# Performance work log

Measured on AMD Instinct MI355X. Metric: run time of the kernel, lower is better.

## Reference

```python
import jax, jax.numpy as jnp
import numpy as np

MAX_DEPTH = 7
DEPTH_SIZES = [4 ** d for d in range(1, MAX_DEPTH + 1)]  # nodes per depth
N_NODES = sum(DEPTH_SIZES)  # 21844
N_TIMES = 48
HIDDEN = 1024
ENC_DIM = 256
B, S = 128, 32


def setup_inputs() -> dict:
    key = jax.random.key(0)
    k = jax.random.split(key, 6)
    return {
        "prefix_embedding": jax.random.normal(k[0], (B, S, HIDDEN), dtype=jnp.float32),
        "emb_matrix": jax.random.normal(k[1], (N_NODES, ENC_DIM), dtype=jnp.float32) * 0.02,
        "W_key": jax.random.normal(k[2], (HIDDEN, ENC_DIM), dtype=jnp.float32) * (1.0 / np.sqrt(ENC_DIM)),
        "b_key": jax.random.normal(k[3], (HIDDEN,), dtype=jnp.float32) * 0.01,
        "W_time": jax.random.normal(k[4], (N_TIMES, HIDDEN), dtype=jnp.float32) * (1.0 / np.sqrt(HIDDEN)),
        "b_time": jax.random.normal(k[5], (N_TIMES,), dtype=jnp.float32) * 0.01,
    }


def reference(prefix_embedding, emb_matrix, W_key, b_key, W_time, b_time):
    # keys = embedding_to_key(make_embedding_matrix(...)): [N_NODES, HIDDEN]
    keys = emb_matrix @ W_key.T + b_key
    # bmm(prefix [B,S,H], keys^T): keys identical across batch -> shared einsum
    scores = jnp.einsum("bsh,nh->bsn", prefix_embedding, keys)  # [B,S,N_NODES]
    # multitask: per-depth gather of the contiguous node block + log_softmax
    locations = []
    off = 0
    for n in DEPTH_SIZES:
        locations.append(jax.nn.log_softmax(scores[..., off:off + n], axis=-1))
        off += n
    time = jax.nn.log_softmax(prefix_embedding @ W_time.T + b_time, axis=-1)  # [B,S,N_TIMES]
    return tuple(locations) + (time,)
```

## Files before the change

kernel.cpp:

```cpp
#include <hip/hip_runtime.h>

#define NNODES 21844
#define ENC 256
#define HID 1024
#define ROWS 4096
#define NTIMES 48

typedef __attribute__((ext_vector_type(8))) short bf16x8;
typedef __attribute__((ext_vector_type(8))) unsigned short u16x8;
typedef __attribute__((ext_vector_type(4))) float f32x4;

__device__ const int g_off[8] = {0, 4, 20, 84, 340, 1364, 5460, 21844};

__device__ inline unsigned short f2bf(float f) {
  unsigned int u = __float_as_uint(f);
  u += 0x7FFF + ((u >> 16) & 1);
  return (unsigned short)(u >> 16);
}

__device__ inline int depth_of(int c) {
  return (c >= 4) + (c >= 20) + (c >= 84) + (c >= 340) + (c >= 1364) + (c >= 5460);
}

__global__ __launch_bounds__(256) void prep(const float* __restrict__ prefix,
                                            const float* __restrict__ emb,
                                            const float* __restrict__ Wk,
                                            const float* __restrict__ Wt,
                                            unsigned short* __restrict__ Pb16,
                                            unsigned short* __restrict__ Eb,
                                            unsigned short* __restrict__ WkT,
                                            float* __restrict__ WtT,
                                            float* __restrict__ S) {
  int bid = blockIdx.x, tid = threadIdx.x;
  if (bid < 4096) {
    int i = bid * 256 + tid;
    float4 v = reinterpret_cast<const float4*>(prefix)[i];
    ushort4 o; o.x = f2bf(v.x); o.y = f2bf(v.y); o.z = f2bf(v.z); o.w = f2bf(v.w);
    reinterpret_cast<ushort4*>(Pb16)[i] = o;
  } else if (bid < 9557) {
    int i = (bid - 4096) * 256 + tid;
    float4 v = reinterpret_cast<const float4*>(emb)[i];
    ushort4 o; o.x = f2bf(v.x); o.y = f2bf(v.y); o.z = f2bf(v.z); o.w = f2bf(v.w);
    reinterpret_cast<ushort4*>(Eb)[i] = o;
  } else if (bid < 10581) {
    int i = (bid - 9557) * 256 + tid;
    int e = i >> 10, h = i & 1023;
    WkT[i] = f2bf(Wk[h * ENC + e]);
  } else if (bid < 10773) {
    int i = (bid - 10581) * 256 + tid;
    int k = i / NTIMES, c = i % NTIMES;
    WtT[i] = Wt[c * HID + k];
  } else {
    int i = (bid - 10773) * 256 + tid;
    reinterpret_cast<float4*>(S)[i] = float4{0.f, 0.f, 0.f, 0.f};
  }
}

__global__ __launch_bounds__(256) void p2_mfma(const unsigned short* __restrict__ Ab,
                                               const unsigned short* __restrict__ Bb,
                                               unsigned short* __restrict__ P2) {
  int lane = threadIdx.x & 63, w = threadIdx.x >> 6;
  int lr = lane & 15, lg = lane >> 4;
  int m0 = blockIdx.y * 64 + w * 16;
  int nb = blockIdx.x * 64;
  f32x4 acc[4];
#pragma unroll
  for (int n = 0; n < 4; ++n) acc[n] = f32x4{0.f, 0.f, 0.f, 0.f};
  const unsigned short* Ap = Ab + (long)(m0 + lr) * HID + lg * 8;
  for (int kk = 0; kk < 32; ++kk) {
    bf16x8 a = *reinterpret_cast<const bf16x8*>(Ap + kk * 32);
#pragma unroll
    for (int n = 0; n < 4; ++n) {
      bf16x8 b = *reinterpret_cast<const bf16x8*>(Bb + (long)(nb + n * 16 + lr) * HID + kk * 32 + lg * 8);
      acc[n] = __builtin_amdgcn_mfma_f32_16x16x32_bf16(a, b, acc[n], 0, 0, 0);
    }
  }
#pragma unroll
  for (int n = 0; n < 4; ++n)
#pragma unroll
    for (int j = 0; j < 4; ++j)
      P2[(m0 + lg * 4 + j) * ENC + nb + n * 16 + lr] = f2bf(acc[n][j]);
}

template <int BF16S>
__global__ __launch_bounds__(256) void gemm_stash(const unsigned short* __restrict__ P2,
                                                  const unsigned short* __restrict__ E,
                                                  unsigned short* __restrict__ stash,
                                                  float* __restrict__ outp,
                                                  float* __restrict__ S) {
  __shared__ unsigned short SH[2][2][128 * 64];
  int tid = threadIdx.x;
  int lane = tid & 63, w = tid >> 6;
  int lr = lane & 15, lg = lane >> 4;
  int wr = w >> 1, wc = w & 1;
  int m0 = blockIdx.x * 128, n0 = blockIdx.y * 128;
  int rr = tid >> 3, c8 = tid & 7;

  f32x4 acc[4][4];
#pragma unroll
  for (int m = 0; m < 4; ++m)
#pragma unroll
    for (int n = 0; n < 4; ++n) acc[m][n] = f32x4{0.f, 0.f, 0.f, 0.f};

#define STAGE(buf, kt)                                                                    \
  _Pragma("unroll") for (int r = 0; r < 4; ++r) {                                         \
    const unsigned short* ga = P2 + (long)(m0 + r * 32 + rr) * ENC + (kt) * 64 + c8 * 8;  \
    __builtin_amdgcn_global_load_lds(                                                     \
        (const __attribute__((address_space(1))) unsigned int*)ga,                        \
        (__attribute__((address_space(3))) unsigned int*)(&SH[buf][0][r * 2048 + w * 512]), \
        16, 0, 0);                                                                        \
    int er = n0 + r * 32 + rr;                                                            \
    if (er > NNODES - 1) er = NNODES - 1;                                                 \
    const unsigned short* gb = E + (long)er * ENC + (kt) * 64 + c8 * 8;                   \
    __builtin_amdgcn_global_load_lds(                                                     \
        (const __attribute__((address_space(1))) unsigned int*)gb,                        \
        (__attribute__((address_space(3))) unsigned int*)(&SH[buf][1][r * 2048 + w * 512]), \
        16, 0, 0);                                                                        \
  }

  STAGE(0, 0)
  __syncthreads();
  for (int kt = 0; kt < 4; ++kt) {
    int cur = kt & 1;
    if (kt < 3) { STAGE(cur ^ 1, kt + 1) }
    const unsigned short* As = &SH[cur][0][0];
    const unsigned short* Bs = &SH[cur][1][0];
#pragma unroll
    for (int kk = 0; kk < 2; ++kk) {
      bf16x8 a[4], b[4];
#pragma unroll
      for (int m = 0; m < 4; ++m)
        a[m] = *reinterpret_cast<const bf16x8*>(As + (wr * 64 + m * 16 + lr) * 64 + kk * 32 + lg * 8);
#pragma unroll
      for (int n = 0; n < 4; ++n)
        b[n] = *reinterpret_cast<const bf16x8*>(Bs + (wc * 64 + n * 16 + lr) * 64 + kk * 32 + lg * 8);
#pragma unroll
      for (int m = 0; m < 4; ++m)
#pragma unroll
        for (int n = 0; n < 4; ++n)
          acc[m][n] = __builtin_amdgcn_mfma_f32_16x16x32_bf16(a[m], b[n], acc[m][n], 0, 0, 0);
    }
    __syncthreads();
  }
#undef STAGE

  int rbase = m0 + wr * 64 + lg * 4;
  int hstart = n0 + wc * 64;
#pragma unroll
  for (int n = 0; n < 4; ++n) {
    int gc = hstart + n * 16 + lr;
    if (gc < NNODES) {
      int d = depth_of(gc);
      long ob = ((long)g_off[d] << 12) + (gc - g_off[d]);
      int sh = 2 * (d + 1);
#pragma unroll
      for (int m = 0; m < 4; ++m)
#pragma unroll
        for (int j = 0; j < 4; ++j) {
          int row = rbase + m * 16 + j;
          long idx = ob + ((long)row << sh);
          if (BF16S) stash[idx] = f2bf(acc[m][n][j]);
          else       outp[idx]  = acc[m][n][j];
        }
    }
  }
  int dlo = depth_of(hstart);
  int hend = hstart + 63; if (hend > NNODES - 1) hend = NNODES - 1;
  int dhi = depth_of(hend);
  int cd[4];
#pragma unroll
  for (int n = 0; n < 4; ++n) {
    int gc = hstart + n * 16 + lr;
    cd[n] = (gc < NNODES) ? depth_of(gc) : 99;
  }
#pragma unroll
  for (int m = 0; m < 4; ++m)
#pragma unroll
    for (int n = 0; n < 4; ++n)
#pragma unroll
      for (int j = 0; j < 4; ++j) acc[m][n][j] = __expf(acc[m][n][j]);
  for (int dt = dlo; dt <= dhi; ++dt) {
#pragma unroll
    for (int m = 0; m < 4; ++m) {
      float s[4] = {0.f, 0.f, 0.f, 0.f};
#pragma unroll
      for (int n = 0; n < 4; ++n) {
        bool use = (cd[n] == dt);
#pragma unroll
        for (int j = 0; j < 4; ++j) s[j] += use ? acc[m][n][j] : 0.f;
      }
#pragma unroll
      for (int j = 0; j < 4; ++j)
#pragma unroll
        for (int o = 1; o < 16; o <<= 1) s[j] += __shfl_xor(s[j], o);
      if (lr == 0) {
#pragma unroll
        for (int j = 0; j < 4; ++j)
          atomicAdd(&S[dt * ROWS + rbase + m * 16 + j], s[j]);
      }
    }
  }
}

template <int BF16S>
__global__ __launch_bounds__(256) void sub_write(const unsigned short* __restrict__ stash,
                                                 const float* __restrict__ S,
                                                 float* __restrict__ out,
                                                 const float* __restrict__ prefix,
                                                 const float* __restrict__ WtT,
                                                 const float* __restrict__ bt) {
  if (blockIdx.x >= 43688) {
    int lane = threadIdx.x & 63;
    int row = (blockIdx.x - 43688) * 4 + (threadIdx.x >> 6);
    const float4* pr = reinterpret_cast<const float4*>(prefix + (long)row * HID);
    float acc = -3.4e38f;
    if (lane < NTIMES) {
      float a = 0.f;
#pragma unroll 4
      for (int q = 0; q < HID / 4; ++q) {
        float4 pv = pr[q];
        const float* wrow = WtT + q * 4 * NTIMES;
        a += pv.x * wrow[lane] + pv.y * wrow[NTIMES + lane] +
             pv.z * wrow[2 * NTIMES + lane] + pv.w * wrow[3 * NTIMES + lane];
      }
      acc = a + bt[lane];
    }
    float m = acc;
#pragma unroll
    for (int d = 32; d; d >>= 1) m = fmaxf(m, __shfl_xor(m, d));
    float e = (lane < NTIMES) ? __expf(acc - m) : 0.f;
    float s = e;
#pragma unroll
    for (int d = 32; d; d >>= 1) s += __shfl_xor(s, d);
    if (lane < NTIMES)
      __builtin_nontemporal_store(acc - m - __logf(s), out + 89473024 + row * NTIMES + lane);
    return;
  }
  long base = (long)blockIdx.x * 2048 + threadIdx.x * 8;
  int d = (base >= 16384) + (base >= 81920) + (base >= 344064) +
          (base >= 1392640) + (base >= 5586944) + (base >= 22364160);
  long bd = (d == 0) ? 0L : (d == 1) ? 16384L : (d == 2) ? 81920L : (d == 3) ? 344064L
          : (d == 4) ? 1392640L : (d == 5) ? 5586944L : 22364160L;
  long rel = base - bd;
  const float* sp = S + d * ROWS;
  float v[8];
  if (BF16S) {
    u16x8 u = *reinterpret_cast<const u16x8*>(stash + base);
#pragma unroll
    for (int j = 0; j < 8; ++j) v[j] = __uint_as_float((unsigned)(unsigned short)u[j] << 16);
  } else {
    float4 a = reinterpret_cast<const float4*>(out + base)[0];
    float4 b = reinterpret_cast<const float4*>(out + base)[1];
    v[0] = a.x; v[1] = a.y; v[2] = a.z; v[3] = a.w;
    v[4] = b.x; v[5] = b.y; v[6] = b.z; v[7] = b.w;
  }
  f32x4 o0, o1;
  if (d == 0) {
    int r0 = (int)(rel >> 2);
    float l0 = __logf(sp[r0]), l1 = __logf(sp[r0 + 1]);
    o0 = f32x4{v[0] - l0, v[1] - l0, v[2] - l0, v[3] - l0};
    o1 = f32x4{v[4] - l1, v[5] - l1, v[6] - l1, v[7] - l1};
  } else {
    int row = (int)(rel >> (2 * (d + 1)));
    float l = __logf(sp[row]);
    o0 = f32x4{v[0] - l, v[1] - l, v[2] - l, v[3] - l};
    o1 = f32x4{v[4] - l, v[5] - l, v[6] - l, v[7] - l};
  }
  f32x4* op = reinterpret_cast<f32x4*>(out + base);
  __builtin_nontemporal_store(o0, op);
  __builtin_nontemporal_store(o1, op + 1);
}

extern "C" void kernel_launch(void* const* d_in, const int* in_sizes, int n_in,
                              void* d_out, int out_size, void* d_ws, size_t ws_size,
                              hipStream_t stream) {
  const float* prefix = (const float*)d_in[0];
  const float* emb    = (const float*)d_in[1];
  const float* Wk     = (const float*)d_in[2];
  const float* Wt     = (const float*)d_in[4];
  const float* bt     = (const float*)d_in[5];
  float* out = (float*)d_out;
  char* ws = (char*)d_ws;

  unsigned short* P2    = (unsigned short*)(ws + 0);
  unsigned short* Eb    = (unsigned short*)(ws + 2097152);
  unsigned short* WkT   = (unsigned short*)(ws + 13281280);
  unsigned short* Pb16  = (unsigned short*)(ws + 13805568);
  float*          WtT   = (float*)(ws + 22194176);
  float*          S     = (float*)(ws + 22390784);
  unsigned short* stash = (unsigned short*)(ws + 22505472);
  const size_t WS_NEED_STASH = 22505472UL + 178946048UL;

  bool big = ws_size >= WS_NEED_STASH;

  prep<<<10801, 256, 0, stream>>>(prefix, emb, Wk, Wt, Pb16, Eb, WkT, WtT, S);

  p2_mfma<<<dim3(4, 64), 256, 0, stream>>>(Pb16, WkT, P2);

  if (big) {
    gemm_stash<1><<<dim3(32, 171), 256, 0, stream>>>(P2, Eb, stash, out, S);
    sub_write<1><<<44712, 256, 0, stream>>>(stash, S, out, prefix, WtT, bt);
  } else {
    gemm_stash<0><<<dim3(32, 171), 256, 0, stream>>>(P2, Eb, stash, out, S);
    sub_write<0><<<44712, 256, 0, stream>>>(stash, S, out, prefix, WtT, bt);
  }
}
```

Measured before the change: 362.7 us.

## Stage GEMM tile through LDS for coalesced stash stores; persistent sub_write grid

Measured after the change: 385.0 us. 1.06x slower.

```diff
diff --git a/kernel.cpp b/kernel.cpp
--- a/kernel.cpp
+++ b/kernel.cpp
@@ -8,6 +8,7 @@
 
 typedef __attribute__((ext_vector_type(8))) short bf16x8;
 typedef __attribute__((ext_vector_type(8))) unsigned short u16x8;
+typedef __attribute__((ext_vector_type(4))) unsigned short u16x4;
 typedef __attribute__((ext_vector_type(4))) float f32x4;
 
 __device__ const int g_off[8] = {0, 4, 20, 84, 340, 1364, 5460, 21844};
@@ -144,60 +145,97 @@
   }
 #undef STAGE
 
-  int rbase = m0 + wr * 64 + lg * 4;
-  int hstart = n0 + wc * 64;
-#pragma unroll
-  for (int n = 0; n < 4; ++n) {
-    int gc = hstart + n * 16 + lr;
-    if (gc < NNODES) {
-      int d = depth_of(gc);
-      long ob = ((long)g_off[d] << 12) + (gc - g_off[d]);
-      int sh = 2 * (d + 1);
-#pragma unroll
-      for (int m = 0; m < 4; ++m)
-#pragma unroll
-        for (int j = 0; j < 4; ++j) {
-          int row = rbase + m * 16 + j;
-          long idx = ob + ((long)row << sh);
-          if (BF16S) stash[idx] = f2bf(acc[m][n][j]);
-          else       outp[idx]  = acc[m][n][j];
+  int hend = n0 + 127; if (hend > NNODES - 1) hend = NNODES - 1;
+  int d0 = depth_of(n0), d1 = depth_of(hend);
+  bool fast = BF16S && (d0 == d1) && (d0 >= 3) && (n0 + 128 <= NNODES);
+
+  unsigned short* T = &SH[0][0][0];
+  int rl0 = wr * 64 + lg * 4;
+  int cl0 = wc * 64 + lr;
+#pragma unroll
+  for (int n = 0; n < 4; ++n)
+#pragma unroll
+    for (int m = 0; m < 4; ++m)
+#pragma unroll
+      for (int j = 0; j < 4; ++j) {
+        int rl = rl0 + m * 16 + j, cl = cl0 + n * 16;
+        T[rl * 128 + (cl ^ ((rl & 7) << 3))] = f2bf(acc[m][n][j]);
+      }
+
+  if (!fast) {
+    int rbase = m0 + rl0;
+#pragma unroll
+    for (int n = 0; n < 4; ++n) {
+      int gc = n0 + cl0 + n * 16;
+      if (gc < NNODES) {
+        int d = depth_of(gc);
+        long ob = ((long)g_off[d] << 12) + (gc - g_off[d]);
+        int sh = 2 * (d + 1);
+#pragma unroll
+        for (int m = 0; m < 4; ++m)
+#pragma unroll
+          for (int j = 0; j < 4; ++j) {
+            int row = rbase + m * 16 + j;
+            long idx = ob + ((long)row << sh);
+            if (BF16S) stash[idx] = f2bf(acc[m][n][j]);
+            else       outp[idx]  = acc[m][n][j];
+          }
+      }
+    }
+  }
+
+  {
+    int rbase = m0 + rl0;
+    int hstart = n0 + wc * 64;
+    int dlo = depth_of(hstart);
+    int he2 = hstart + 63; if (he2 > NNODES - 1) he2 = NNODES - 1;
+    int dhi = depth_of(he2);
+    int cd[4];
+#pragma unroll
+    for (int n = 0; n < 4; ++n) {
+      int gc = hstart + n * 16 + lr;
+      cd[n] = (gc < NNODES) ? depth_of(gc) : 99;
+    }
+#pragma unroll
+    for (int m = 0; m < 4; ++m)
+#pragma unroll
+      for (int n = 0; n < 4; ++n)
+#pragma unroll
+        for (int j = 0; j < 4; ++j) acc[m][n][j] = __expf(acc[m][n][j]);
+    for (int dt = dlo; dt <= dhi; ++dt) {
+#pragma unroll
+      for (int m = 0; m < 4; ++m) {
+        float s[4] = {0.f, 0.f, 0.f, 0.f};
+#pragma unroll
+        for (int n = 0; n < 4; ++n) {
+          bool use = (cd[n] == dt);
+#pragma unroll
+          for (int j = 0; j < 4; ++j) s[j] += use ? acc[m][n][j] : 0.f;
         }
-    }
-  }
-  int dlo = depth_of(hstart);
-  int hend = hstart + 63; if (hend > NNODES - 1) hend = NNODES - 1;
-  int dhi = depth_of(hend);
-  int cd[4];
-#pragma unroll
-  for (int n = 0; n < 4; ++n) {
-    int gc = hstart + n * 16 + lr;
-    cd[n] = (gc < NNODES) ? depth_of(gc) : 99;
-  }
-#pragma unroll
-  for (int m = 0; m < 4; ++m)
-#pragma unroll
-    for (int n = 0; n < 4; ++n)
-#pragma unroll
-      for (int j = 0; j < 4; ++j) acc[m][n][j] = __expf(acc[m][n][j]);
-  for (int dt = dlo; dt <= dhi; ++dt) {
-#pragma unroll
-    for (int m = 0; m < 4; ++m) {
-      float s[4] = {0.f, 0.f, 0.f, 0.f};
-#pragma unroll
-      for (int n = 0; n < 4; ++n) {
-        bool use = (cd[n] == dt);
-#pragma unroll
-        for (int j = 0; j < 4; ++j) s[j] += use ? acc[m][n][j] : 0.f;
+#pragma unroll
+        for (int j = 0; j < 4; ++j)
+#pragma unroll
+          for (int o = 1; o < 16; o <<= 1) s[j] += __shfl_xor(s[j], o);
+        if (lr == 0) {
+#pragma unroll
+          for (int j = 0; j < 4; ++j)
+            atomicAdd(&S[dt * ROWS + rbase + m * 16 + j], s[j]);
+        }
       }
-#pragma unroll
-      for (int j = 0; j < 4; ++j)
-#pragma unroll
-        for (int o = 1; o < 16; o <<= 1) s[j] += __shfl_xor(s[j], o);
-      if (lr == 0) {
-#pragma unroll
-        for (int j = 0; j < 4; ++j)
-          atomicAdd(&S[dt * ROWS + rbase + m * 16 + j], s[j]);
-      }
+    }
+  }
+
+  __syncthreads();
+  if (fast) {
+    int off = g_off[d0];
+    long nd = 4L << (2 * d0);
+    int row = tid >> 1, seg = (tid & 1) * 64;
+    long idx = ((long)ROWS) * off + (long)(m0 + row) * nd + (n0 - off) + seg;
+    u16x4* dst = reinterpret_cast<u16x4*>(stash + idx);
+#pragma unroll
+    for (int q = 0; q < 16; ++q) {
+      int col = (seg + q * 4) ^ ((row & 7) << 3);
+      dst[q] = *reinterpret_cast<const u16x4*>(&T[row * 128 + col]);
     }
   }
 }
@@ -209,66 +247,70 @@
                                                  const float* __restrict__ prefix,
                                                  const float* __restrict__ WtT,
                                                  const float* __restrict__ bt) {
-  if (blockIdx.x >= 43688) {
-    int lane = threadIdx.x & 63;
-    int row = (blockIdx.x - 43688) * 4 + (threadIdx.x >> 6);
-    const float4* pr = reinterpret_cast<const float4*>(prefix + (long)row * HID);
-    float acc = -3.4e38f;
-    if (lane < NTIMES) {
-      float a = 0.f;
-#pragma unroll 4
-      for (int q = 0; q < HID / 4; ++q) {
-        float4 pv = pr[q];
-        const float* wrow = WtT + q * 4 * NTIMES;
-        a += pv.x * wrow[lane] + pv.y * wrow[NTIMES + lane] +
-             pv.z * wrow[2 * NTIMES + lane] + pv.w * wrow[3 * NTIMES + lane];
+  int tid = threadIdx.x;
+  if (blockIdx.x < 256) {
+    int lane = tid & 63, w = tid >> 6;
+#pragma unroll
+    for (int r4 = 0; r4 < 4; ++r4) {
+      int row = blockIdx.x * 16 + w * 4 + r4;
+      const float4* pr = reinterpret_cast<const float4*>(prefix + (long)row * HID);
+      float acc = -3.4e38f;
+      if (lane < NTIMES) {
+        float a0 = 0.f, a1 = 0.f, a2 = 0.f, a3 = 0.f;
+        for (int q = 0; q < HID / 4; ++q) {
+          float4 pv = pr[q];
+          const float* wrow = WtT + q * 4 * NTIMES;
+          a0 += pv.x * wrow[lane];
+          a1 += pv.y * wrow[NTIMES + lane];
+          a2 += pv.z * wrow[2 * NTIMES + lane];
+          a3 += pv.w * wrow[3 * NTIMES + lane];
+        }
+        acc = (a0 + a1) + (a2 + a3) + bt[lane];
       }
-      acc = a + bt[lane];
-    }
-    float m = acc;
-#pragma unroll
-    for (int d = 32; d; d >>= 1) m = fmaxf(m, __shfl_xor(m, d));
-    float e = (lane < NTIMES) ? __expf(acc - m) : 0.f;
-    float s = e;
-#pragma unroll
-    for (int d = 32; d; d >>= 1) s += __shfl_xor(s, d);
-    if (lane < NTIMES)
-      __builtin_nontemporal_store(acc - m - __logf(s), out + 89473024 + row * NTIMES + lane);
+      float m = acc;
+#pragma unroll
+      for (int d = 32; d; d >>= 1) m = fmaxf(m, __shfl_xor(m, d));
+      float e = (lane < NTIMES) ? __expf(acc - m) : 0.f;
+      float s = e;
+#pragma unroll
+      for (int d = 32; d; d >>= 1) s += __shfl_xor(s, d);
+      if (lane < NTIMES) out[89473024 + row * NTIMES + lane] = acc - m - __logf(s);
+    }
     return;
   }
-  long base = (long)blockIdx.x * 2048 + threadIdx.x * 8;
-  int d = (base >= 16384) + (base >= 81920) + (base >= 344064) +
-          (base >= 1392640) + (base >= 5586944) + (base >= 22364160);
-  long bd = (d == 0) ? 0L : (d == 1) ? 16384L : (d == 2) ? 81920L : (d == 3) ? 344064L
-          : (d == 4) ? 1392640L : (d == 5) ? 5586944L : 22364160L;
-  long rel = base - bd;
-  const float* sp = S + d * ROWS;
-  float v[8];
-  if (BF16S) {
-    u16x8 u = *reinterpret_cast<const u16x8*>(stash + base);
-#pragma unroll
-    for (int j = 0; j < 8; ++j) v[j] = __uint_as_float((unsigned)(unsigned short)u[j] << 16);
-  } else {
-    float4 a = reinterpret_cast<const float4*>(out + base)[0];
-    float4 b = reinterpret_cast<const float4*>(out + base)[1];
-    v[0] = a.x; v[1] = a.y; v[2] = a.z; v[3] = a.w;
-    v[4] = b.x; v[5] = b.y; v[6] = b.z; v[7] = b.w;
-  }
-  f32x4 o0, o1;
-  if (d == 0) {
-    int r0 = (int)(rel >> 2);
-    float l0 = __logf(sp[r0]), l1 = __logf(sp[r0 + 1]);
-    o0 = f32x4{v[0] - l0, v[1] - l0, v[2] - l0, v[3] - l0};
-    o1 = f32x4{v[4] - l1, v[5] - l1, v[6] - l1, v[7] - l1};
-  } else {
-    int row = (int)(rel >> (2 * (d + 1)));
-    float l = __logf(sp[row]);
-    o0 = f32x4{v[0] - l, v[1] - l, v[2] - l, v[3] - l};
-    o1 = f32x4{v[4] - l, v[5] - l, v[6] - l, v[7] - l};
-  }
-  f32x4* op = reinterpret_cast<f32x4*>(out + base);
-  __builtin_nontemporal_store(o0, op);
-  __builtin_nontemporal_store(o1, op + 1);
+  for (int c = (int)blockIdx.x - 256; c < 43688; c += 2048) {
+    long base = (long)c * 2048 + tid * 8;
+    int d = (c >= 8) + (c >= 40) + (c >= 168) + (c >= 680) + (c >= 2728) + (c >= 10920);
+    long bd = (d == 0) ? 0L : (d == 1) ? 16384L : (d == 2) ? 81920L : (d == 3) ? 344064L
+            : (d == 4) ? 1392640L : (d == 5) ? 5586944L : 22364160L;
+    long rel = base - bd;
+    const float* sp = S + d * ROWS;
+    float v[8];
+    if (BF16S) {
+      u16x8 u = *reinterpret_cast<const u16x8*>(stash + base);
+#pragma unroll
+      for (int j = 0; j < 8; ++j) v[j] = __uint_as_float((unsigned)(unsigned short)u[j] << 16);
+    } else {
+      float4 a = reinterpret_cast<const float4*>(out + base)[0];
+      float4 b = reinterpret_cast<const float4*>(out + base)[1];
+      v[0] = a.x; v[1] = a.y; v[2] = a.z; v[3] = a.w;
+      v[4] = b.x; v[5] = b.y; v[6] = b.z; v[7] = b.w;
+    }
+    float4 o0, o1;
+    if (d == 0) {
+      int r0 = (int)(rel >> 2);
+      float l0 = __logf(sp[r0]), l1 = __logf(sp[r0 + 1]);
+      o0 = float4{v[0] - l0, v[1] - l0, v[2] - l0, v[3] - l0};
+      o1 = float4{v[4] - l1, v[5] - l1, v[6] - l1, v[7] - l1};
+    } else {
+      int row = (int)(rel >> (2 * (d + 1)));
+      float l = __logf(sp[row]);
+      o0 = float4{v[0] - l, v[1] - l, v[2] - l, v[3] - l};
+      o1 = float4{v[4] - l, v[5] - l, v[6] - l, v[7] - l};
+    }
+    reinterpret_cast<float4*>(out + base)[0] = o0;
+    reinterpret_cast<float4*>(out + base)[1] = o1;
+  }
 }
 
 extern "C" void kernel_launch(void* const* d_in, const int* in_sizes, int n_in,
@@ -299,9 +341,9 @@
 
   if (big) {
     gemm_stash<1><<<dim3(32, 171), 256, 0, stream>>>(P2, Eb, stash, out, S);
-    sub_write<1><<<44712, 256, 0, stream>>>(stash, S, out, prefix, WtT, bt);
+    sub_write<1><<<2304, 256, 0, stream>>>(stash, S, out, prefix, WtT, bt);
   } else {
     gemm_stash<0><<<dim3(32, 171), 256, 0, stream>>>(P2, Eb, stash, out, S);
-    sub_write<0><<<44712, 256, 0, stream>>>(stash, S, out, prefix, WtT, bt);
-  }
-}
+    sub_write<0><<<2304, 256, 0, stream>>>(stash, S, out, prefix, WtT, bt);
+  }
+}
```
